# Performance work log

Hardware: AMD Instinct MI355X
Metric: run time of the kernel (lower is better)

## Reference

```python
import jax, jax.numpy as jnp
import numpy as np

N_NODES = 100000
N_GRAPHS = 512


def gcn_conv(x, W, b, src, dst, n):
    # PyG GCNConv: h = x @ W; add self-loops; sym-normalize; scatter-add to dst; + bias
    h = x @ W
    loop = jnp.arange(n, dtype=src.dtype)
    s = jnp.concatenate([src, loop])
    d = jnp.concatenate([dst, loop])
    deg = jax.ops.segment_sum(jnp.ones_like(d, dtype=h.dtype), d, num_segments=n)
    dinv = jnp.where(deg > 0, jax.lax.rsqrt(deg), 0.0)
    norm = dinv[s] * dinv[d]               # [E+N]
    msg = h[s] * norm[:, None]             # gather + scale
    out = jax.ops.segment_sum(msg, d, num_segments=n)
    return out + b


def setup_inputs() -> dict:
    key = jax.random.key(0)
    ks = jax.random.split(key, 12)
    F_in, H, C = 128, 128, 10
    x = jax.random.normal(ks[0], (N_NODES, F_in), dtype=jnp.float32)
    edge_index = jax.random.randint(ks[1], (2, 3200000), 0, N_NODES, dtype=jnp.int64)
    batch = jnp.sort(jax.random.randint(ks[2], (N_NODES,), 0, N_GRAPHS, dtype=jnp.int64))
    def glorot(k, fi, fo):
        s = jnp.sqrt(6.0 / (fi + fo))
        return jax.random.uniform(k, (fi, fo), dtype=jnp.float32, minval=-s, maxval=s)
    return {
        "x": x, "edge_index": edge_index, "batch": batch,
        "W_in": glorot(ks[3], F_in, H), "b_in": jnp.zeros((H,), jnp.float32),
        "W_h0": glorot(ks[4], H, H), "b_h0": jnp.zeros((H,), jnp.float32),
        "W_h1": glorot(ks[5], H, H), "b_h1": jnp.zeros((H,), jnp.float32),
        "W_out": glorot(ks[6], H, C), "b_out": jnp.zeros((C,), jnp.float32),
    }


def reference(x, edge_index, batch, W_in, b_in, W_h0, b_h0, W_h1, b_h1, W_out, b_out):
    src, dst = edge_index[0], edge_index[1]
    n = x.shape[0]
    h = jax.nn.relu(gcn_conv(x, W_in, b_in, src, dst, n))
    h = jax.nn.relu(gcn_conv(h, W_h0, b_h0, src, dst, n))
    h = jax.nn.relu(gcn_conv(h, W_h1, b_h1, src, dst, n))
    h = gcn_conv(h, W_out, b_out, src, dst, n)
    # global_mean_pool over graph ids
    sums = jax.ops.segment_sum(h, batch, num_segments=N_GRAPHS)
    cnts = jax.ops.segment_sum(jnp.ones((n,), h.dtype), batch, num_segments=N_GRAPHS)
    pooled = sums / jnp.maximum(cnts, 1.0)[:, None]
    return jax.nn.log_softmax(pooled, axis=-1)
```

## Files before the change

kernel.cpp:

```cpp
#include <hip/hip_runtime.h>
#include <math.h>

#define TPB 256
#define MAXDEG 80
#define SHIFT 8
#define BNODES 256
#define CAP 10240
#define EPB 4096
#define LSTR 136
#define NCHUNK 13

typedef short bf16x8 __attribute__((ext_vector_type(8)));
typedef float f32x4 __attribute__((ext_vector_type(4)));

__device__ inline unsigned short f2bf(float f) {
    unsigned u = __float_as_uint(f);
    return (unsigned short)((u + 0x7fffu + ((u >> 16) & 1u)) >> 16);
}
__device__ inline float bflo(unsigned u) { return __uint_as_float(u << 16); }
__device__ inline float bfhi(unsigned u) { return __uint_as_float(u & 0xffff0000u); }


__global__ __launch_bounds__(TPB) void p1_k(const int* __restrict__ src,
                                            const int* __restrict__ dst,
                                            int* __restrict__ gbcnt,
                                            int* __restrict__ buckets, int E, int nb) {
    __shared__ int hist[512];
    __shared__ int lcur[512];
    int tid = threadIdx.x;
    for (int b = tid; b < nb; b += TPB) hist[b] = 0;
    __syncthreads();
    int e0 = blockIdx.x * EPB;
    int m = E - e0; if (m > EPB) m = EPB;
    for (int i = tid; i < m; i += TPB)
        atomicAdd(&hist[dst[e0 + i] >> SHIFT], 1);
    __syncthreads();
    for (int b = tid; b < nb; b += TPB) {
        int h = hist[b];
        lcur[b] = h ? atomicAdd(&gbcnt[b], h) : 0;
    }
    __syncthreads();
    for (int i = tid; i < m; i += TPB) {
        int d = dst[e0 + i];
        int s = src[e0 + i];
        int b = d >> SHIFT;
        int pos = atomicAdd(&lcur[b], 1);
        if (pos < CAP) buckets[(size_t)b * CAP + pos] = (s << SHIFT) | (d & (BNODES - 1));
    }
}


__global__ __launch_bounds__(TPB) void p2_k(const int* __restrict__ gbcnt,
                                            const int* __restrict__ buckets,
                                            int* __restrict__ csr,
                                            int* __restrict__ deg,
                                            float* __restrict__ dinv, int n, int nb,
                                            const float* __restrict__ W0,
                                            const float* __restrict__ W1,
                                            const float* __restrict__ W2,
                                            const float* __restrict__ W3,
                                            unsigned short* __restrict__ T0,
                                            unsigned short* __restrict__ T1,
                                            unsigned short* __restrict__ T2,
                                            unsigned short* __restrict__ T3,
                                            float* __restrict__ pool,
                                            int* __restrict__ cnt, int ng) {
    int b = blockIdx.x, tid = threadIdx.x;
    if (b >= nb) {
        int widx = b - nb;
        if (widx < 3) {
            const float* W = widx == 0 ? W0 : (widx == 1 ? W1 : W2);
            unsigned short* T = widx == 0 ? T0 : (widx == 1 ? T1 : T2);
            for (int idx = tid; idx < 16384; idx += TPB) {
                int nn = idx >> 7, kk = idx & 127;
                T[idx] = f2bf(W[kk * 128 + nn]);
            }
        } else {
            for (int idx = tid; idx < 2048; idx += TPB) {
                int nn = idx >> 7, kk = idx & 127;
                T3[idx] = nn < 10 ? f2bf(W3[kk * 10 + nn]) : (unsigned short)0;
            }
            for (int i = tid; i < ng * 10; i += TPB) pool[i] = 0.f;
            for (int i = tid; i < ng; i += TPB) cnt[i] = 0;
        }
        return;
    }
    __shared__ int lc[BNODES][NCHUNK];
    for (int i = tid; i < BNODES * NCHUNK; i += TPB) ((int*)lc)[i] = 0;
    __syncthreads();
    int m = gbcnt[b]; if (m > CAP) m = CAP;
    const int* bp = buckets + (size_t)b * CAP;
    int vb = b << SHIFT;
    for (int i = tid; i < m; i += TPB) {
        int rec = bp[i];
        atomicAdd(&lc[rec & (BNODES - 1)][(rec >> SHIFT) >> 13], 1);
    }
    __syncthreads();
    {
        int run = 0;
#pragma unroll
        for (int c = 0; c < NCHUNK; c++) { int t = lc[tid][c]; lc[tid][c] = run; run += t; }
        int v = vb + tid;
        if (v < n) {
            deg[v] = run < MAXDEG ? run : MAXDEG;
            dinv[v] = rsqrtf((float)(run + 1));
        }
    }
    __syncthreads();
    for (int i = tid; i < m; i += TPB) {
        int rec = bp[i];
        int dl = rec & (BNODES - 1);
        int s = rec >> SHIFT;
        int pos = atomicAdd(&lc[dl][s >> 13], 1);
        if (pos < MAXDEG) csr[(size_t)(vb + dl) * MAXDEG + pos] = s;
    }
}


__device__ __forceinline__ void mfma_tile(const unsigned short* Hs,
                                          const unsigned short* __restrict__ WT,
                                          const float* __restrict__ dinv,
                                          unsigned short* __restrict__ gout,
                                          int vb, int n, int w, int l) {
    f32x4 acc[2][8];
#pragma unroll
    for (int a = 0; a < 2; a++)
#pragma unroll
        for (int b = 0; b < 8; b++)
#pragma unroll
            for (int j = 0; j < 4; j++) acc[a][b][j] = 0.f;
    const int quad = l >> 4, lm = l & 15;
    const int mrow0 = w * 32;
#pragma unroll
    for (int ks = 0; ks < 4; ks++) {
        bf16x8 a0 = *(const bf16x8*)(Hs + (mrow0 + lm) * LSTR + ks * 32 + quad * 8);
        bf16x8 a1 = *(const bf16x8*)(Hs + (mrow0 + 16 + lm) * LSTR + ks * 32 + quad * 8);
#pragma unroll
        for (int nt = 0; nt < 8; nt++) {
            bf16x8 bf = *(const bf16x8*)(WT + (size_t)(nt * 16 + lm) * 128 + ks * 32 + quad * 8);
            acc[0][nt] = __builtin_amdgcn_mfma_f32_16x16x32_bf16(a0, bf, acc[0][nt], 0, 0, 0);
            acc[1][nt] = __builtin_amdgcn_mfma_f32_16x16x32_bf16(a1, bf, acc[1][nt], 0, 0, 0);
        }
    }
#pragma unroll
    for (int mt = 0; mt < 2; mt++) {
#pragma unroll
        for (int j = 0; j < 4; j++) {
            int r = vb + mrow0 + mt * 16 + quad * 4 + j;
            if (r < n) {
                float s = dinv[r];
#pragma unroll
                for (int nt = 0; nt < 8; nt++)
                    gout[(size_t)r * 128 + nt * 16 + lm] = f2bf(acc[mt][nt][j] * s);
            }
        }
    }
}


__global__ __launch_bounds__(256) void gemm_f32in(const float* __restrict__ x,
                                                  const unsigned short* __restrict__ WT,
                                                  const float* __restrict__ dinv,
                                                  unsigned short* __restrict__ gout, int n) {
    __shared__ unsigned short Hs[128 * LSTR];
    int tid = threadIdx.x;
    int vb = blockIdx.x * 128;
    for (int i = tid; i < 8192; i += 256) {
        int row = i >> 6, cw = i & 63;
        int gr = vb + row; if (gr > n - 1) gr = n - 1;
        float2 xv = *(const float2*)(x + (size_t)gr * 128 + cw * 2);
        unsigned pk = ((unsigned)f2bf(xv.y) << 16) | f2bf(xv.x);
        *(unsigned*)(Hs + row * LSTR + cw * 2) = pk;
    }
    __syncthreads();
    mfma_tile(Hs, WT, dinv, gout, vb, n, tid >> 6, tid & 63);
}


__global__ __launch_bounds__(256) void gemm_bf16in(const unsigned* __restrict__ hin,
                                                   const unsigned short* __restrict__ WT,
                                                   const float* __restrict__ dinv,
                                                   unsigned short* __restrict__ gout, int n) {
    __shared__ unsigned short Hs[128 * LSTR];
    int tid = threadIdx.x;
    int vb = blockIdx.x * 128;
    for (int i = tid; i < 8192; i += 256) {
        int row = i >> 6, cw = i & 63;
        int gr = vb + row; if (gr > n - 1) gr = n - 1;
        *(unsigned*)(Hs + row * LSTR + cw * 2) = hin[(size_t)gr * 64 + cw];
    }
    __syncthreads();
    mfma_tile(Hs, WT, dinv, gout, vb, n, tid >> 6, tid & 63);
}


__global__ __launch_bounds__(256) void thin_mfma(const unsigned* __restrict__ hin,
                                                 const unsigned short* __restrict__ WT3,
                                                 const float* __restrict__ dinv,
                                                 unsigned* __restrict__ g4u, int n) {
    __shared__ unsigned short Hs[128 * LSTR];
    int tid = threadIdx.x;
    int vb = blockIdx.x * 128;
    for (int i = tid; i < 8192; i += 256) {
        int row = i >> 6, cw = i & 63;
        int gr = vb + row; if (gr > n - 1) gr = n - 1;
        *(unsigned*)(Hs + row * LSTR + cw * 2) = hin[(size_t)gr * 64 + cw];
    }
    __syncthreads();
    int w = tid >> 6, l = tid & 63;
    int quad = l >> 4, lm = l & 15;
    int mrow0 = w * 32;
    f32x4 acc[2];
#pragma unroll
    for (int a = 0; a < 2; a++)
#pragma unroll
        for (int j = 0; j < 4; j++) acc[a][j] = 0.f;
#pragma unroll
    for (int ks = 0; ks < 4; ks++) {
        bf16x8 a0 = *(const bf16x8*)(Hs + (mrow0 + lm) * LSTR + ks * 32 + quad * 8);
        bf16x8 a1 = *(const bf16x8*)(Hs + (mrow0 + 16 + lm) * LSTR + ks * 32 + quad * 8);
        bf16x8 bf = *(const bf16x8*)(WT3 + (size_t)lm * 128 + ks * 32 + quad * 8);
        acc[0] = __builtin_amdgcn_mfma_f32_16x16x32_bf16(a0, bf, acc[0], 0, 0, 0);
        acc[1] = __builtin_amdgcn_mfma_f32_16x16x32_bf16(a1, bf, acc[1], 0, 0, 0);
    }
#pragma unroll
    for (int mt = 0; mt < 2; mt++) {
#pragma unroll
        for (int j = 0; j < 4; j++) {
            float self = acc[mt][j];
            float part = __shfl_down(self, 1, 64);
            int r = vb + mrow0 + mt * 16 + quad * 4 + j;
            if ((lm & 1) == 0 && lm < 10 && r < n) {
                float s = dinv[r];
                g4u[(size_t)r * 5 + (lm >> 1)] =
                    ((unsigned)f2bf(part * s) << 16) | f2bf(self * s);
            }
        }
    }
}


__global__ __launch_bounds__(256) void aggb_k(const unsigned* __restrict__ g,
                                              const float* __restrict__ dinv,
                                              const int* __restrict__ deg,
                                              const int* __restrict__ csr,
                                              const float* __restrict__ bias,
                                              unsigned* __restrict__ hout, int n) {
    int w = __builtin_amdgcn_readfirstlane((int)(threadIdx.x >> 6));
    int l = threadIdx.x & 63;
    int v = blockIdx.x * 4 + w;
    if (v >= n) return;
    unsigned u = g[(size_t)v * 64 + l];
    float acc0 = bflo(u), acc1 = bfhi(u);
    const int* cp = csr + (size_t)v * MAXDEG;
    int d = deg[v];
    int e = 0;
    for (; e + 16 <= d; e += 16) {
        unsigned uu[16];
#pragma unroll
        for (int j = 0; j < 16; j++) uu[j] = g[(size_t)cp[e + j] * 64 + l];
#pragma unroll
        for (int j = 0; j < 16; j++) { acc0 += bflo(uu[j]); acc1 += bfhi(uu[j]); }
    }
    for (; e + 4 <= d; e += 4) {
        unsigned uu[4];
#pragma unroll
        for (int j = 0; j < 4; j++) uu[j] = g[(size_t)cp[e + j] * 64 + l];
#pragma unroll
        for (int j = 0; j < 4; j++) { acc0 += bflo(uu[j]); acc1 += bfhi(uu[j]); }
    }
    for (; e < d; e++) {
        unsigned ux = g[(size_t)cp[e] * 64 + l];
        acc0 += bflo(ux); acc1 += bfhi(ux);
    }
    float2 bb = *(const float2*)(bias + 2 * l);
    float s = dinv[v];
    float o0 = fmaxf(s * acc0 + bb.x, 0.f);
    float o1 = fmaxf(s * acc1 + bb.y, 0.f);
    hout[(size_t)v * 64 + l] = ((unsigned)f2bf(o1) << 16) | f2bf(o0);
}


__global__ __launch_bounds__(TPB) void agg_thin_bf(const unsigned* __restrict__ g4u,
                                                   const float* __restrict__ dinv,
                                                   const int* __restrict__ deg,
                                                   const int* __restrict__ csr,
                                                   const float* __restrict__ bias,
                                                   float* __restrict__ out, int n) {
    int idx = blockIdx.x * TPB + threadIdx.x;
    if (idx >= n * 5) return;
    int v = idx / 5, t = idx - v * 5;
    unsigned u = g4u[(size_t)v * 5 + t];
    float acc0 = bflo(u), acc1 = bfhi(u);
    const int* cp = csr + (size_t)v * MAXDEG;
    int d = deg[v];
    int e = 0;
    for (; e + 4 <= d; e += 4) {
        unsigned u0 = g4u[(size_t)cp[e] * 5 + t];
        unsigned u1 = g4u[(size_t)cp[e + 1] * 5 + t];
        unsigned u2 = g4u[(size_t)cp[e + 2] * 5 + t];
        unsigned u3 = g4u[(size_t)cp[e + 3] * 5 + t];
        acc0 += (bflo(u0) + bflo(u1)) + (bflo(u2) + bflo(u3));
        acc1 += (bfhi(u0) + bfhi(u1)) + (bfhi(u2) + bfhi(u3));
    }
    for (; e < d; e++) {
        unsigned ux = g4u[(size_t)cp[e] * 5 + t];
        acc0 += bflo(ux); acc1 += bfhi(ux);
    }
    float s = dinv[v];
    out[(size_t)v * 10 + 2 * t]     = s * acc0 + bias[2 * t];
    out[(size_t)v * 10 + 2 * t + 1] = s * acc1 + bias[2 * t + 1];
}


#define POOL_SPAN 8

__global__ __launch_bounds__(TPB) void pool_k(const float* __restrict__ h,
                                              const int* __restrict__ batch,
                                              float* __restrict__ pool, int* __restrict__ cnt, int n) {
    __shared__ float lp[POOL_SPAN][10];
    __shared__ int lc[POOL_SPAN];
    __shared__ int g0;
    int tid = threadIdx.x;
    int v = blockIdx.x * TPB + tid;
    if (tid == 0) {
        int first = blockIdx.x * TPB;
        if (first > n - 1) first = n - 1;
        g0 = batch[first];
    }
    if (tid < POOL_SPAN) lc[tid] = 0;
    if (tid < POOL_SPAN * 10) lp[tid / 10][tid % 10] = 0.f;
    __syncthreads();
    if (v < n) {
        int gi = batch[v];
        int o = gi - g0;
        if (o < POOL_SPAN) {
            atomicAdd(&lc[o], 1);
#pragma unroll
            for (int c = 0; c < 10; c++) atomicAdd(&lp[o][c], h[(size_t)v * 10 + c]);
        } else {
            atomicAdd(&cnt[gi], 1);
#pragma unroll
            for (int c = 0; c < 10; c++) atomicAdd(&pool[gi * 10 + c], h[(size_t)v * 10 + c]);
        }
    }
    __syncthreads();
    if (tid < POOL_SPAN) {
        if (lc[tid] > 0) atomicAdd(&cnt[g0 + tid], lc[tid]);
    }
    if (tid < POOL_SPAN * 10) {
        int o = tid / 10, c = tid % 10;
        if (lc[o] > 0) atomicAdd(&pool[(g0 + o) * 10 + c], lp[o][c]);
    }
}

__global__ __launch_bounds__(TPB) void final_k(const float* __restrict__ pool,
                                               const int* __restrict__ cnt,
                                               float* __restrict__ out, int ng) {
    int gi = blockIdx.x * TPB + threadIdx.x;
    if (gi >= ng) return;
    float cn = fmaxf((float)cnt[gi], 1.f);
    float x[10];
    float m = -1e30f;
#pragma unroll
    for (int c = 0; c < 10; c++) {
        x[c] = pool[gi * 10 + c] / cn;
        m = fmaxf(m, x[c]);
    }
    float s = 0.f;
#pragma unroll
    for (int c = 0; c < 10; c++) s += expf(x[c] - m);
    float l = logf(s);
#pragma unroll
    for (int c = 0; c < 10; c++) out[gi * 10 + c] = x[c] - m - l;
}


extern "C" void kernel_launch(void* const* d_in, const int* in_sizes, int n_in,
                              void* d_out, int out_size, void* d_ws, size_t ws_size,
                              hipStream_t stream) {
    const float* x    = (const float*)d_in[0];
    const int*   ei   = (const int*)d_in[1];
    const int*   batch= (const int*)d_in[2];
    const float* W_in = (const float*)d_in[3];
    const float* b_in = (const float*)d_in[4];
    const float* W_h0 = (const float*)d_in[5];
    const float* b_h0 = (const float*)d_in[6];
    const float* W_h1 = (const float*)d_in[7];
    const float* b_h1 = (const float*)d_in[8];
    const float* W_out= (const float*)d_in[9];
    const float* b_out= (const float*)d_in[10];

    const int n  = in_sizes[2];
    const int E  = in_sizes[1] / 2;
    const int ng = out_size / 10;
    const int nb = (n + BNODES - 1) >> SHIFT;

    char* p = (char*)d_ws;
    auto carve = [&](size_t bytes) { void* r = (void*)p; p += (bytes + 255) & ~(size_t)255; return r; };
    int*            deg    = (int*)           carve((size_t)n * 4);
    float*          dinv   = (float*)         carve((size_t)n * 4);
    int*            gbcnt  = (int*)           carve((size_t)nb * 4);
    int*            buckets= (int*)           carve((size_t)nb * CAP * 4);
    int*            csr    = (int*)           carve((size_t)n * MAXDEG * 4);
    unsigned*       G      = (unsigned*)      carve((size_t)n * 64 * 4);
    unsigned*       H      = (unsigned*)      carve((size_t)n * 64 * 4);
    unsigned short* WT0    = (unsigned short*)carve(16384 * 2);
    unsigned short* WT1    = (unsigned short*)carve(16384 * 2);
    unsigned short* WT2    = (unsigned short*)carve(16384 * 2);
    unsigned short* WT3    = (unsigned short*)carve(2048 * 2);
    unsigned*       g4u    = (unsigned*)      carve((size_t)n * 5 * 4);
    float*          h10    = (float*)         carve((size_t)n * 10 * 4);
    float*          pool   = (float*)         carve((size_t)ng * 10 * 4);
    int*            cnt    = (int*)           carve((size_t)ng * 4);

    (void)hipMemsetAsync(gbcnt, 0, (size_t)nb * 4, stream);

    const int gN = (n + TPB - 1) / TPB;
    const int gP1 = (E + EPB - 1) / EPB;
    const int gG = (n + 127) / 128;
    const int gA4 = (n + 3) / 4;

    p1_k<<<gP1, TPB, 0, stream>>>(ei, ei + E, gbcnt, buckets, E, nb);
    p2_k<<<nb + 4, TPB, 0, stream>>>(gbcnt, buckets, csr, deg, dinv, n, nb,
                                     W_in, W_h0, W_h1, W_out, WT0, WT1, WT2, WT3,
                                     pool, cnt, ng);

    gemm_f32in<<<gG, 256, 0, stream>>>(x, WT0, dinv, (unsigned short*)G, n);
    aggb_k<<<gA4, 256, 0, stream>>>(G, dinv, deg, csr, b_in, H, n);
    gemm_bf16in<<<gG, 256, 0, stream>>>(H, WT1, dinv, (unsigned short*)G, n);
    aggb_k<<<gA4, 256, 0, stream>>>(G, dinv, deg, csr, b_h0, H, n);
    gemm_bf16in<<<gG, 256, 0, stream>>>(H, WT2, dinv, (unsigned short*)G, n);
    aggb_k<<<gA4, 256, 0, stream>>>(G, dinv, deg, csr, b_h1, H, n);
    thin_mfma<<<gG, 256, 0, stream>>>(H, WT3, dinv, g4u, n);
    agg_thin_bf<<<(n * 5 + TPB - 1) / TPB, TPB, 0, stream>>>(g4u, dinv, deg, csr, b_out, h10, n);
    pool_k<<<gN, TPB, 0, stream>>>(h10, batch, pool, cnt, n);
    final_k<<<(ng + TPB - 1) / TPB, TPB, 0, stream>>>(pool, cnt, (float*)d_out, ng);
}
```

Baseline: 663.2 us.

## Split feature matrices into column quarters for cache-local aggregation; simplify CSR build

The 128-wide bf16 feature matrices are stored as four column-major slabs of 32 features each. Aggregation runs as four passes, one slab per blockIdx range, with 16 lanes per node. Each pass gathers from a 3.2 MB slab instead of the full 12.8 MB matrix, so the random neighbour gathers are more likely to hit L2/MALL. The CSR build drops the chunked counting sort and fills rows with a single atomic pass, so neighbour order within a row is no longer sorted by source chunk. Fewer bytes are fetched per gather request, and the summation order changes slightly.

```diff
diff --git a/kernel.cpp b/kernel.cpp
--- a/kernel.cpp
+++ b/kernel.cpp
@@ -8,7 +8,6 @@
 #define CAP 10240
 #define EPB 4096
 #define LSTR 136
-#define NCHUNK 13
 
 typedef short bf16x8 __attribute__((ext_vector_type(8)));
 typedef float f32x4 __attribute__((ext_vector_type(4)));
@@ -19,6 +18,7 @@
 }
 __device__ inline float bflo(unsigned u) { return __uint_as_float(u << 16); }
 __device__ inline float bfhi(unsigned u) { return __uint_as_float(u & 0xffff0000u); }
+
 
 
 __global__ __launch_bounds__(TPB) void p1_k(const int* __restrict__ src,
@@ -85,34 +85,24 @@
         }
         return;
     }
-    __shared__ int lc[BNODES][NCHUNK];
-    for (int i = tid; i < BNODES * NCHUNK; i += TPB) ((int*)lc)[i] = 0;
+    __shared__ int lcnt[BNODES];
+    lcnt[tid] = 0;
     __syncthreads();
     int m = gbcnt[b]; if (m > CAP) m = CAP;
     const int* bp = buckets + (size_t)b * CAP;
     int vb = b << SHIFT;
     for (int i = tid; i < m; i += TPB) {
         int rec = bp[i];
-        atomicAdd(&lc[rec & (BNODES - 1)][(rec >> SHIFT) >> 13], 1);
-    }
-    __syncthreads();
-    {
-        int run = 0;
-#pragma unroll
-        for (int c = 0; c < NCHUNK; c++) { int t = lc[tid][c]; lc[tid][c] = run; run += t; }
-        int v = vb + tid;
-        if (v < n) {
-            deg[v] = run < MAXDEG ? run : MAXDEG;
-            dinv[v] = rsqrtf((float)(run + 1));
-        }
-    }
-    __syncthreads();
-    for (int i = tid; i < m; i += TPB) {
-        int rec = bp[i];
         int dl = rec & (BNODES - 1);
-        int s = rec >> SHIFT;
-        int pos = atomicAdd(&lc[dl][s >> 13], 1);
-        if (pos < MAXDEG) csr[(size_t)(vb + dl) * MAXDEG + pos] = s;
+        int pos = atomicAdd(&lcnt[dl], 1);
+        if (pos < MAXDEG) csr[(size_t)(vb + dl) * MAXDEG + pos] = rec >> SHIFT;
+    }
+    __syncthreads();
+    int v = vb + tid;
+    if (v < n) {
+        int c = lcnt[tid];
+        deg[v] = c < MAXDEG ? c : MAXDEG;
+        dinv[v] = rsqrtf((float)(c + 1));
     }
 }
 
@@ -150,8 +140,10 @@
             if (r < n) {
                 float s = dinv[r];
 #pragma unroll
-                for (int nt = 0; nt < 8; nt++)
-                    gout[(size_t)r * 128 + nt * 16 + lm] = f2bf(acc[mt][nt][j] * s);
+                for (int nt = 0; nt < 8; nt++) {
+                    size_t base = ((size_t)((nt >> 1) * n + r)) * 32;
+                    gout[base + (nt & 1) * 16 + lm] = f2bf(acc[mt][nt][j] * s);
+                }
             }
         }
     }
@@ -187,7 +179,8 @@
     for (int i = tid; i < 8192; i += 256) {
         int row = i >> 6, cw = i & 63;
         int gr = vb + row; if (gr > n - 1) gr = n - 1;
-        *(unsigned*)(Hs + row * LSTR + cw * 2) = hin[(size_t)gr * 64 + cw];
+        *(unsigned*)(Hs + row * LSTR + cw * 2) =
+            hin[((size_t)((cw >> 4) * n + gr)) * 16 + (cw & 15)];
     }
     __syncthreads();
     mfma_tile(Hs, WT, dinv, gout, vb, n, tid >> 6, tid & 63);
@@ -204,7 +197,8 @@
     for (int i = tid; i < 8192; i += 256) {
         int row = i >> 6, cw = i & 63;
         int gr = vb + row; if (gr > n - 1) gr = n - 1;
-        *(unsigned*)(Hs + row * LSTR + cw * 2) = hin[(size_t)gr * 64 + cw];
+        *(unsigned*)(Hs + row * LSTR + cw * 2) =
+            hin[((size_t)((cw >> 4) * n + gr)) * 16 + (cw & 15)];
     }
     __syncthreads();
     int w = tid >> 6, l = tid & 63;
@@ -240,44 +234,49 @@
 }
 
 
-__global__ __launch_bounds__(256) void aggb_k(const unsigned* __restrict__ g,
+__global__ __launch_bounds__(256) void aggq_k(const unsigned* __restrict__ G,
                                               const float* __restrict__ dinv,
                                               const int* __restrict__ deg,
                                               const int* __restrict__ csr,
                                               const float* __restrict__ bias,
-                                              unsigned* __restrict__ hout, int n) {
-    int w = __builtin_amdgcn_readfirstlane((int)(threadIdx.x >> 6));
-    int l = threadIdx.x & 63;
-    int v = blockIdx.x * 4 + w;
+                                              unsigned* __restrict__ H, int n, int nblk) {
+    int q = blockIdx.x / nblk;
+    int blk = blockIdx.x - q * nblk;
+    int w = threadIdx.x >> 6, l = threadIdx.x & 63;
+    int sub = l >> 4, t = l & 15;
+    int v = blk * 16 + w * 4 + sub;
     if (v >= n) return;
-    unsigned u = g[(size_t)v * 64 + l];
-    float acc0 = bflo(u), acc1 = bfhi(u);
+    const unsigned* Gq = G + (size_t)q * n * 16;
+    unsigned u = Gq[(size_t)v * 16 + t];
+    float a0 = bflo(u), a1 = bfhi(u);
     const int* cp = csr + (size_t)v * MAXDEG;
     int d = deg[v];
     int e = 0;
-    for (; e + 16 <= d; e += 16) {
-        unsigned uu[16];
-#pragma unroll
-        for (int j = 0; j < 16; j++) uu[j] = g[(size_t)cp[e + j] * 64 + l];
-#pragma unroll
-        for (int j = 0; j < 16; j++) { acc0 += bflo(uu[j]); acc1 += bfhi(uu[j]); }
-    }
-    for (; e + 4 <= d; e += 4) {
-        unsigned uu[4];
-#pragma unroll
-        for (int j = 0; j < 4; j++) uu[j] = g[(size_t)cp[e + j] * 64 + l];
-#pragma unroll
-        for (int j = 0; j < 4; j++) { acc0 += bflo(uu[j]); acc1 += bfhi(uu[j]); }
+    for (; e + 8 <= d; e += 8) {
+        int s0 = cp[e], s1 = cp[e + 1], s2 = cp[e + 2], s3 = cp[e + 3];
+        int s4 = cp[e + 4], s5 = cp[e + 5], s6 = cp[e + 6], s7 = cp[e + 7];
+        unsigned u0 = Gq[(size_t)s0 * 16 + t];
+        unsigned u1 = Gq[(size_t)s1 * 16 + t];
+        unsigned u2 = Gq[(size_t)s2 * 16 + t];
+        unsigned u3 = Gq[(size_t)s3 * 16 + t];
+        unsigned u4 = Gq[(size_t)s4 * 16 + t];
+        unsigned u5 = Gq[(size_t)s5 * 16 + t];
+        unsigned u6 = Gq[(size_t)s6 * 16 + t];
+        unsigned u7 = Gq[(size_t)s7 * 16 + t];
+        a0 += (bflo(u0) + bflo(u1)) + (bflo(u2) + bflo(u3))
+            + (bflo(u4) + bflo(u5)) + (bflo(u6) + bflo(u7));
+        a1 += (bfhi(u0) + bfhi(u1)) + (bfhi(u2) + bfhi(u3))
+            + (bfhi(u4) + bfhi(u5)) + (bfhi(u6) + bfhi(u7));
     }
     for (; e < d; e++) {
-        unsigned ux = g[(size_t)cp[e] * 64 + l];
-        acc0 += bflo(ux); acc1 += bfhi(ux);
-    }
-    float2 bb = *(const float2*)(bias + 2 * l);
+        unsigned ux = Gq[(size_t)cp[e] * 16 + t];
+        a0 += bflo(ux); a1 += bfhi(ux);
+    }
+    float2 bb = *(const float2*)(bias + q * 32 + 2 * t);
     float s = dinv[v];
-    float o0 = fmaxf(s * acc0 + bb.x, 0.f);
-    float o1 = fmaxf(s * acc1 + bb.y, 0.f);
-    hout[(size_t)v * 64 + l] = ((unsigned)f2bf(o1) << 16) | f2bf(o0);
+    float o0 = fmaxf(s * a0 + bb.x, 0.f);
+    float o1 = fmaxf(s * a1 + bb.y, 0.f);
+    H[((size_t)q * n + v) * 16 + t] = ((unsigned)f2bf(o1) << 16) | f2bf(o0);
 }
 
 
@@ -419,7 +418,8 @@
     const int gN = (n + TPB - 1) / TPB;
     const int gP1 = (E + EPB - 1) / EPB;
     const int gG = (n + 127) / 128;
-    const int gA4 = (n + 3) / 4;
+    const int nblk = (n + 15) / 16;
+    const int gAq = 4 * nblk;
 
     p1_k<<<gP1, TPB, 0, stream>>>(ei, ei + E, gbcnt, buckets, E, nb);
     p2_k<<<nb + 4, TPB, 0, stream>>>(gbcnt, buckets, csr, deg, dinv, n, nb,
@@ -427,11 +427,11 @@
                                      pool, cnt, ng);
 
     gemm_f32in<<<gG, 256, 0, stream>>>(x, WT0, dinv, (unsigned short*)G, n);
-    aggb_k<<<gA4, 256, 0, stream>>>(G, dinv, deg, csr, b_in, H, n);
+    aggq_k<<<gAq, 256, 0, stream>>>(G, dinv, deg, csr, b_in, H, n, nblk);
     gemm_bf16in<<<gG, 256, 0, stream>>>(H, WT1, dinv, (unsigned short*)G, n);
-    aggb_k<<<gA4, 256, 0, stream>>>(G, dinv, deg, csr, b_h0, H, n);
+    aggq_k<<<gAq, 256, 0, stream>>>(G, dinv, deg, csr, b_h0, H, n, nblk);
     gemm_bf16in<<<gG, 256, 0, stream>>>(H, WT2, dinv, (unsigned short*)G, n);
-    aggb_k<<<gA4, 256, 0, stream>>>(G, dinv, deg, csr, b_h1, H, n);
+    aggq_k<<<gAq, 256, 0, stream>>>(G, dinv, deg, csr, b_h1, H, n, nblk);
     thin_mfma<<<gG, 256, 0, stream>>>(H, WT3, dinv, g4u, n);
     agg_thin_bf<<<(n * 5 + TPB - 1) / TPB, TPB, 0, stream>>>(g4u, dinv, deg, csr, b_out, h10, n);
     pool_k<<<gN, TPB, 0, stream>>>(h10, batch, pool, cnt, n);
```

Result: slower. 762.1 us (+14.9%).

## Build CSR from per-block sub-buckets, fuse thin aggregation with pooling

Applied to the files above, without the earlier changes.

The edge bucketing kernel now writes each block's edges into fixed-size per-(bucket, block) slots plus a count matrix. This removes the global atomic counter, the per-block histogram pass and the memset. The CSR kernel makes a single pass over those slots and no longer groups each node's neighbours by source chunk, which may reduce cache locality in the later gathers. The final 10-wide aggregation is fused with mean-pool accumulation, dropping the h10 intermediate and one launch. The big aggregation loop is also re-unrolled to 8 with a tree-summed accumulation. Any (bucket, block) slot holding more than QB edges silently drops edges.

```diff
diff --git a/kernel.cpp b/kernel.cpp
--- a/kernel.cpp
+++ b/kernel.cpp
@@ -5,10 +5,9 @@
 #define MAXDEG 80
 #define SHIFT 8
 #define BNODES 256
-#define CAP 10240
 #define EPB 4096
+#define QB 32
 #define LSTR 136
-#define NCHUNK 13
 
 typedef short bf16x8 __attribute__((ext_vector_type(8)));
 typedef float f32x4 __attribute__((ext_vector_type(4)));
@@ -23,38 +22,36 @@
 
 __global__ __launch_bounds__(TPB) void p1_k(const int* __restrict__ src,
                                             const int* __restrict__ dst,
-                                            int* __restrict__ gbcnt,
-                                            int* __restrict__ buckets, int E, int nb) {
-    __shared__ int hist[512];
+                                            int* __restrict__ cntmat,
+                                            int* __restrict__ buckets,
+                                            int E, int nb, int nblk1) {
     __shared__ int lcur[512];
-    int tid = threadIdx.x;
-    for (int b = tid; b < nb; b += TPB) hist[b] = 0;
-    __syncthreads();
-    int e0 = blockIdx.x * EPB;
+    int tid = threadIdx.x, blk = blockIdx.x;
+    for (int b = tid; b < nb; b += TPB) lcur[b] = 0;
+    __syncthreads();
+    int e0 = blk * EPB;
     int m = E - e0; if (m > EPB) m = EPB;
-    for (int i = tid; i < m; i += TPB)
-        atomicAdd(&hist[dst[e0 + i] >> SHIFT], 1);
-    __syncthreads();
-    for (int b = tid; b < nb; b += TPB) {
-        int h = hist[b];
-        lcur[b] = h ? atomicAdd(&gbcnt[b], h) : 0;
-    }
-    __syncthreads();
     for (int i = tid; i < m; i += TPB) {
         int d = dst[e0 + i];
         int s = src[e0 + i];
         int b = d >> SHIFT;
         int pos = atomicAdd(&lcur[b], 1);
-        if (pos < CAP) buckets[(size_t)b * CAP + pos] = (s << SHIFT) | (d & (BNODES - 1));
-    }
-}
-
-
-__global__ __launch_bounds__(TPB) void p2_k(const int* __restrict__ gbcnt,
+        if (pos < QB)
+            buckets[((size_t)b * nblk1 + blk) * QB + pos] = (s << SHIFT) | (d & (BNODES - 1));
+    }
+    __syncthreads();
+    for (int b = tid; b < nb; b += TPB) {
+        int c = lcur[b];
+        cntmat[blk * nb + b] = c < QB ? c : QB;
+    }
+}
+
+
+__global__ __launch_bounds__(TPB) void p2_k(const int* __restrict__ cntmat,
                                             const int* __restrict__ buckets,
                                             int* __restrict__ csr,
                                             int* __restrict__ deg,
-                                            float* __restrict__ dinv, int n, int nb,
+                                            float* __restrict__ dinv, int n, int nb, int nblk1,
                                             const float* __restrict__ W0,
                                             const float* __restrict__ W1,
                                             const float* __restrict__ W2,
@@ -85,34 +82,30 @@
         }
         return;
     }
-    __shared__ int lc[BNODES][NCHUNK];
-    for (int i = tid; i < BNODES * NCHUNK; i += TPB) ((int*)lc)[i] = 0;
-    __syncthreads();
-    int m = gbcnt[b]; if (m > CAP) m = CAP;
-    const int* bp = buckets + (size_t)b * CAP;
+    __shared__ int lcnt[BNODES];
+    __shared__ int cnts[784];
+    lcnt[tid] = 0;
+    for (int blk = tid; blk < nblk1; blk += TPB) cnts[blk] = cntmat[blk * nb + b];
+    __syncthreads();
+    const int* bp = buckets + (size_t)b * nblk1 * QB;
     int vb = b << SHIFT;
-    for (int i = tid; i < m; i += TPB) {
-        int rec = bp[i];
-        atomicAdd(&lc[rec & (BNODES - 1)][(rec >> SHIFT) >> 13], 1);
-    }
-    __syncthreads();
-    {
-        int run = 0;
-#pragma unroll
-        for (int c = 0; c < NCHUNK; c++) { int t = lc[tid][c]; lc[tid][c] = run; run += t; }
-        int v = vb + tid;
-        if (v < n) {
-            deg[v] = run < MAXDEG ? run : MAXDEG;
-            dinv[v] = rsqrtf((float)(run + 1));
-        }
-    }
-    __syncthreads();
-    for (int i = tid; i < m; i += TPB) {
-        int rec = bp[i];
-        int dl = rec & (BNODES - 1);
-        int s = rec >> SHIFT;
-        int pos = atomicAdd(&lc[dl][s >> 13], 1);
-        if (pos < MAXDEG) csr[(size_t)(vb + dl) * MAXDEG + pos] = s;
+    int tot = nblk1 * QB;
+    for (int j = tid; j < tot; j += TPB) {
+        int blk = j / QB;
+        int i = j - blk * QB;
+        if (i < cnts[blk]) {
+            int rec = bp[(size_t)blk * QB + i];
+            int dl = rec & (BNODES - 1);
+            int pos = atomicAdd(&lcnt[dl], 1);
+            if (pos < MAXDEG) csr[(size_t)(vb + dl) * MAXDEG + pos] = rec >> SHIFT;
+        }
+    }
+    __syncthreads();
+    int v = vb + tid;
+    if (v < n) {
+        int c = lcnt[tid];
+        deg[v] = c < MAXDEG ? c : MAXDEG;
+        dinv[v] = rsqrtf((float)(c + 1));
     }
 }
 
@@ -255,19 +248,21 @@
     const int* cp = csr + (size_t)v * MAXDEG;
     int d = deg[v];
     int e = 0;
-    for (; e + 16 <= d; e += 16) {
-        unsigned uu[16];
-#pragma unroll
-        for (int j = 0; j < 16; j++) uu[j] = g[(size_t)cp[e + j] * 64 + l];
-#pragma unroll
-        for (int j = 0; j < 16; j++) { acc0 += bflo(uu[j]); acc1 += bfhi(uu[j]); }
-    }
-    for (; e + 4 <= d; e += 4) {
-        unsigned uu[4];
-#pragma unroll
-        for (int j = 0; j < 4; j++) uu[j] = g[(size_t)cp[e + j] * 64 + l];
-#pragma unroll
-        for (int j = 0; j < 4; j++) { acc0 += bflo(uu[j]); acc1 += bfhi(uu[j]); }
+    for (; e + 8 <= d; e += 8) {
+        int s0 = cp[e], s1 = cp[e + 1], s2 = cp[e + 2], s3 = cp[e + 3];
+        int s4 = cp[e + 4], s5 = cp[e + 5], s6 = cp[e + 6], s7 = cp[e + 7];
+        unsigned u0 = g[(size_t)s0 * 64 + l];
+        unsigned u1 = g[(size_t)s1 * 64 + l];
+        unsigned u2 = g[(size_t)s2 * 64 + l];
+        unsigned u3 = g[(size_t)s3 * 64 + l];
+        unsigned u4 = g[(size_t)s4 * 64 + l];
+        unsigned u5 = g[(size_t)s5 * 64 + l];
+        unsigned u6 = g[(size_t)s6 * 64 + l];
+        unsigned u7 = g[(size_t)s7 * 64 + l];
+        acc0 += (bflo(u0) + bflo(u1)) + (bflo(u2) + bflo(u3))
+              + (bflo(u4) + bflo(u5)) + (bflo(u6) + bflo(u7));
+        acc1 += (bfhi(u0) + bfhi(u1)) + (bfhi(u2) + bfhi(u3))
+              + (bfhi(u4) + bfhi(u5)) + (bfhi(u6) + bfhi(u7));
     }
     for (; e < d; e++) {
         unsigned ux = g[(size_t)cp[e] * 64 + l];
@@ -281,76 +276,70 @@
 }
 
 
-__global__ __launch_bounds__(TPB) void agg_thin_bf(const unsigned* __restrict__ g4u,
-                                                   const float* __restrict__ dinv,
-                                                   const int* __restrict__ deg,
-                                                   const int* __restrict__ csr,
-                                                   const float* __restrict__ bias,
-                                                   float* __restrict__ out, int n) {
-    int idx = blockIdx.x * TPB + threadIdx.x;
-    if (idx >= n * 5) return;
-    int v = idx / 5, t = idx - v * 5;
-    unsigned u = g4u[(size_t)v * 5 + t];
-    float acc0 = bflo(u), acc1 = bfhi(u);
-    const int* cp = csr + (size_t)v * MAXDEG;
-    int d = deg[v];
-    int e = 0;
-    for (; e + 4 <= d; e += 4) {
-        unsigned u0 = g4u[(size_t)cp[e] * 5 + t];
-        unsigned u1 = g4u[(size_t)cp[e + 1] * 5 + t];
-        unsigned u2 = g4u[(size_t)cp[e + 2] * 5 + t];
-        unsigned u3 = g4u[(size_t)cp[e + 3] * 5 + t];
-        acc0 += (bflo(u0) + bflo(u1)) + (bflo(u2) + bflo(u3));
-        acc1 += (bfhi(u0) + bfhi(u1)) + (bfhi(u2) + bfhi(u3));
-    }
-    for (; e < d; e++) {
-        unsigned ux = g4u[(size_t)cp[e] * 5 + t];
-        acc0 += bflo(ux); acc1 += bfhi(ux);
-    }
-    float s = dinv[v];
-    out[(size_t)v * 10 + 2 * t]     = s * acc0 + bias[2 * t];
-    out[(size_t)v * 10 + 2 * t + 1] = s * acc1 + bias[2 * t + 1];
-}
-
-
 #define POOL_SPAN 8
 
-__global__ __launch_bounds__(TPB) void pool_k(const float* __restrict__ h,
-                                              const int* __restrict__ batch,
-                                              float* __restrict__ pool, int* __restrict__ cnt, int n) {
+__global__ __launch_bounds__(TPB) void agg_thin_pool(const unsigned* __restrict__ g4u,
+                                                     const float* __restrict__ dinv,
+                                                     const int* __restrict__ deg,
+                                                     const int* __restrict__ csr,
+                                                     const float* __restrict__ bias,
+                                                     const int* __restrict__ batch,
+                                                     float* __restrict__ pool,
+                                                     int* __restrict__ cnt, int n) {
     __shared__ float lp[POOL_SPAN][10];
     __shared__ int lc[POOL_SPAN];
-    __shared__ int g0;
+    __shared__ int g0s;
     int tid = threadIdx.x;
-    int v = blockIdx.x * TPB + tid;
+    int q = tid / 5, t = tid - q * 5;
+    int v = blockIdx.x * 50 + q;
     if (tid == 0) {
-        int first = blockIdx.x * TPB;
-        if (first > n - 1) first = n - 1;
-        g0 = batch[first];
+        int f = blockIdx.x * 50;
+        if (f > n - 1) f = n - 1;
+        g0s = batch[f];
     }
     if (tid < POOL_SPAN) lc[tid] = 0;
     if (tid < POOL_SPAN * 10) lp[tid / 10][tid % 10] = 0.f;
     __syncthreads();
-    if (v < n) {
+    if (tid < 250 && v < n) {
+        unsigned u = g4u[(size_t)v * 5 + t];
+        float acc0 = bflo(u), acc1 = bfhi(u);
+        const int* cp = csr + (size_t)v * MAXDEG;
+        int d = deg[v];
+        int e = 0;
+        for (; e + 4 <= d; e += 4) {
+            unsigned u0 = g4u[(size_t)cp[e] * 5 + t];
+            unsigned u1 = g4u[(size_t)cp[e + 1] * 5 + t];
+            unsigned u2 = g4u[(size_t)cp[e + 2] * 5 + t];
+            unsigned u3 = g4u[(size_t)cp[e + 3] * 5 + t];
+            acc0 += (bflo(u0) + bflo(u1)) + (bflo(u2) + bflo(u3));
+            acc1 += (bfhi(u0) + bfhi(u1)) + (bfhi(u2) + bfhi(u3));
+        }
+        for (; e < d; e++) {
+            unsigned ux = g4u[(size_t)cp[e] * 5 + t];
+            acc0 += bflo(ux); acc1 += bfhi(ux);
+        }
+        float s = dinv[v];
+        float o0 = s * acc0 + bias[2 * t];
+        float o1 = s * acc1 + bias[2 * t + 1];
         int gi = batch[v];
-        int o = gi - g0;
+        int o = gi - g0s;
         if (o < POOL_SPAN) {
-            atomicAdd(&lc[o], 1);
-#pragma unroll
-            for (int c = 0; c < 10; c++) atomicAdd(&lp[o][c], h[(size_t)v * 10 + c]);
+            if (t == 0) atomicAdd(&lc[o], 1);
+            atomicAdd(&lp[o][2 * t], o0);
+            atomicAdd(&lp[o][2 * t + 1], o1);
         } else {
-            atomicAdd(&cnt[gi], 1);
-#pragma unroll
-            for (int c = 0; c < 10; c++) atomicAdd(&pool[gi * 10 + c], h[(size_t)v * 10 + c]);
+            if (t == 0) atomicAdd(&cnt[gi], 1);
+            atomicAdd(&pool[gi * 10 + 2 * t], o0);
+            atomicAdd(&pool[gi * 10 + 2 * t + 1], o1);
         }
     }
     __syncthreads();
     if (tid < POOL_SPAN) {
-        if (lc[tid] > 0) atomicAdd(&cnt[g0 + tid], lc[tid]);
+        if (lc[tid] > 0) atomicAdd(&cnt[g0s + tid], lc[tid]);
     }
     if (tid < POOL_SPAN * 10) {
         int o = tid / 10, c = tid % 10;
-        if (lc[o] > 0) atomicAdd(&pool[(g0 + o) * 10 + c], lp[o][c]);
+        if (lc[o] > 0) atomicAdd(&pool[(g0s + o) * 10 + c], lp[o][c]);
     }
 }
 
@@ -395,13 +384,14 @@
     const int E  = in_sizes[1] / 2;
     const int ng = out_size / 10;
     const int nb = (n + BNODES - 1) >> SHIFT;
+    const int nblk1 = (E + EPB - 1) / EPB;
 
     char* p = (char*)d_ws;
     auto carve = [&](size_t bytes) { void* r = (void*)p; p += (bytes + 255) & ~(size_t)255; return r; };
     int*            deg    = (int*)           carve((size_t)n * 4);
     float*          dinv   = (float*)         carve((size_t)n * 4);
-    int*            gbcnt  = (int*)           carve((size_t)nb * 4);
-    int*            buckets= (int*)           carve((size_t)nb * CAP * 4);
+    int*            cntmat = (int*)           carve((size_t)nblk1 * nb * 4);
+    int*            buckets= (int*)           carve((size_t)nb * nblk1 * QB * 4);
     int*            csr    = (int*)           carve((size_t)n * MAXDEG * 4);
     unsigned*       G      = (unsigned*)      carve((size_t)n * 64 * 4);
     unsigned*       H      = (unsigned*)      carve((size_t)n * 64 * 4);
@@ -410,19 +400,14 @@
     unsigned short* WT2    = (unsigned short*)carve(16384 * 2);
     unsigned short* WT3    = (unsigned short*)carve(2048 * 2);
     unsigned*       g4u    = (unsigned*)      carve((size_t)n * 5 * 4);
-    float*          h10    = (float*)         carve((size_t)n * 10 * 4);
     float*          pool   = (float*)         carve((size_t)ng * 10 * 4);
     int*            cnt    = (int*)           carve((size_t)ng * 4);
 
-    (void)hipMemsetAsync(gbcnt, 0, (size_t)nb * 4, stream);
-
-    const int gN = (n + TPB - 1) / TPB;
-    const int gP1 = (E + EPB - 1) / EPB;
     const int gG = (n + 127) / 128;
     const int gA4 = (n + 3) / 4;
 
-    p1_k<<<gP1, TPB, 0, stream>>>(ei, ei + E, gbcnt, buckets, E, nb);
-    p2_k<<<nb + 4, TPB, 0, stream>>>(gbcnt, buckets, csr, deg, dinv, n, nb,
+    p1_k<<<nblk1, TPB, 0, stream>>>(ei, ei + E, cntmat, buckets, E, nb, nblk1);
+    p2_k<<<nb + 4, TPB, 0, stream>>>(cntmat, buckets, csr, deg, dinv, n, nb, nblk1,
                                      W_in, W_h0, W_h1, W_out, WT0, WT1, WT2, WT3,
                                      pool, cnt, ng);
 
@@ -433,7 +418,6 @@
     gemm_bf16in<<<gG, 256, 0, stream>>>(H, WT2, dinv, (unsigned short*)G, n);
     aggb_k<<<gA4, 256, 0, stream>>>(G, dinv, deg, csr, b_h1, H, n);
     thin_mfma<<<gG, 256, 0, stream>>>(H, WT3, dinv, g4u, n);
-    agg_thin_bf<<<(n * 5 + TPB - 1) / TPB, TPB, 0, stream>>>(g4u, dinv, deg, csr, b_out, h10, n);
-    pool_k<<<gN, TPB, 0, stream>>>(h10, batch, pool, cnt, n);
+    agg_thin_pool<<<(n + 49) / 50, TPB, 0, stream>>>(g4u, dinv, deg, csr, b_out, batch, pool, cnt, n);
     final_k<<<(ng + TPB - 1) / TPB, TPB, 0, stream>>>(pool, cnt, (float*)d_out, ng);
 }
```

Measured after the change: 687.3 us. +3.6%, slower.
